# Optimization experiments

Measured on AMD Instinct MI355X. Metric: run time of the kernel, lower is better.

Reference implementation:

```python
import jax, jax.numpy as jnp
import numpy as np

N, E = 50000, 800000
S, V, RBF_DIM = 128, 16, 16
RBF_DMAX = 20.0
MSG_NORM = 10.0
EPS = 1e-8
DVH_M = V + 1            # message GVP: dim_vectors_in = V + 1 (edge direction appended), dim_h = max(17,16) = 17
FIN_M = S + RBF_DIM      # message GVP scalar input = node scalars + rbf(dist)
DVH_U = 2 * V            # update GVP: dim_vectors_in = 2V (node + aggregated), dim_h = 32
FIN_U = 2 * S


def _rbf(D):
    # [E] -> [E, RBF_DIM], matches torch _rbf with D_min=0, D_max=20, D_count=16
    D_mu = jnp.linspace(0.0, RBF_DMAX, RBF_DIM)
    D_sigma = RBF_DMAX / RBF_DIM
    return jnp.exp(-(((D[:, None] - D_mu[None, :]) / D_sigma) ** 2))


def _gvp(s, v, Wh, Wu, Wf, bf, Wg, bg):
    # s: [n, F_in], v: [n, V_in, 3]; faithful to GVP.forward with sigmoid vector gating
    Vh = jnp.einsum('nvc,vh->nhc', v, Wh)          # [n, H, 3]
    Vu = jnp.einsum('nhc,ho->noc', Vh, Wu)         # [n, V_out, 3]
    sh = jnp.sqrt(jnp.clip(jnp.sum(Vh * Vh, -1), EPS))  # _norm_no_nan
    feats_out = jax.nn.silu(jnp.concatenate([s, sh], -1) @ Wf + bf)
    gate = jax.nn.sigmoid(feats_out @ Wg + bg)[..., None]
    return feats_out, gate * Vu


def _gvp_layernorm(s, v, gamma, beta):
    mu = jnp.mean(s, -1, keepdims=True)
    var = jnp.mean((s - mu) ** 2, -1, keepdims=True)
    s_out = (s - mu) / jnp.sqrt(var + 1e-5) * gamma + beta
    vn = jnp.clip(jnp.sum(v * v, -1, keepdims=True), EPS)        # [N, V, 1]
    vn = jnp.sqrt(jnp.mean(vn, -2, keepdims=True) + 1e-5) + 1e-5  # [N, 1, 1]
    return s_out, v / vn


def setup_inputs() -> dict:
    key = jax.random.key(0)
    ks = jax.random.split(key, 14)
    rn = lambda k, shp, sc: (jax.random.normal(k, shp, dtype=jnp.float32) * sc)
    inp = {
        's': rn(ks[0], (N, S), 1.0),
        'v': rn(ks[1], (N, V, 3), 1.0),
        'x': rn(ks[2], (N, 3), 5.0),
        # message GVP params
        'Wh_m': rn(ks[3], (DVH_M, DVH_M), 1.0 / np.sqrt(DVH_M)),
        'Wu_m': rn(ks[4], (DVH_M, V), 1.0 / np.sqrt(DVH_M)),
        'Wf_m': rn(ks[5], (DVH_M + FIN_M, S), 1.0 / np.sqrt(DVH_M + FIN_M)),
        'bf_m': jnp.zeros((S,), jnp.float32),
        'Wg_m': rn(ks[6], (S, V), 1.0 / np.sqrt(S)),
        'bg_m': jnp.zeros((V,), jnp.float32),
        # update GVP params
        'Wh_u': rn(ks[7], (DVH_U, DVH_U), 1.0 / np.sqrt(DVH_U)),
        'Wu_u': rn(ks[8], (DVH_U, V), 1.0 / np.sqrt(DVH_U)),
        'Wf_u': rn(ks[9], (DVH_U + FIN_U, S), 1.0 / np.sqrt(DVH_U + FIN_U)),
        'bf_u': jnp.zeros((S,), jnp.float32),
        'Wg_u': rn(ks[10], (S, V), 1.0 / np.sqrt(S)),
        'bg_u': jnp.zeros((V,), jnp.float32),
        # layernorm
        'ln_g': jnp.ones((S,), jnp.float32),
        'ln_b': jnp.zeros((S,), jnp.float32),
        'edge_index': jax.random.randint(ks[11], (2, E), 0, N),
    }
    return inp


def reference(s, v, x, Wh_m, Wu_m, Wf_m, bf_m, Wg_m, bg_m,
              Wh_u, Wu_u, Wf_u, bf_u, Wg_u, bg_u, ln_g, ln_b, edge_index):
    src, dst = edge_index[0], edge_index[1]
    # gather + geometric edge features
    dx = x[dst] - x[src]                                   # [E, 3]
    dist = jnp.sqrt(jnp.clip(jnp.sum(dx * dx, -1), EPS))    # [E]
    unit = dx / dist[:, None]
    v_in = jnp.concatenate([v[src], unit[:, None, :]], 1)   # [E, V+1, 3]
    s_in = jnp.concatenate([s[src], _rbf(dist)], -1)        # [E, S+RBF]
    # message GVP
    ms, mv = _gvp(s_in, v_in, Wh_m, Wu_m, Wf_m, bf_m, Wg_m, bg_m)
    # scatter-reduce + message norm
    agg_s = jax.ops.segment_sum(ms, dst, num_segments=N) / MSG_NORM   # [N, S]
    agg_v = jax.ops.segment_sum(mv, dst, num_segments=N) / MSG_NORM   # [N, V, 3]
    # update GVP on concatenated node + aggregated messages
    us, uv = _gvp(jnp.concatenate([s, agg_s], -1), jnp.concatenate([v, agg_v], 1),
                  Wh_u, Wu_u, Wf_u, bf_u, Wg_u, bg_u)
    # residual + GVPLayerNorm
    return _gvp_layernorm(s + us, v + uv, ln_g, ln_b)
```

## Files before the change

kernel.cpp:

```cpp
#include <hip/hip_runtime.h>
#include <hip/hip_bf16.h>
#include <math.h>

#define N_NODES 50000
#define E_EDGES 800000
#define S_DIM 128
#define V_DIM 16
#define HM 17
#define KM 161
#define HU 32
#define KU 288

#define EB 32
#define LDA 164
#define NB 32
#define LDA2 292

__device__ __forceinline__ float bf2f(unsigned short u) {
    union { unsigned int i; float f; } w; w.i = ((unsigned int)u) << 16; return w.f;
}
__device__ __forceinline__ unsigned short f2bf(float f) {
    union { float f; unsigned int i; } w; w.f = f;
    unsigned int x = w.i;
    x += 0x7fff + ((x >> 16) & 1);
    return (unsigned short)(x >> 16);
}
__device__ __forceinline__ float silu_f(float x) { return x / (1.f + __expf(-x)); }
__device__ __forceinline__ float sigm_f(float x) { return 1.f / (1.f + __expf(-x)); }
__device__ __forceinline__ float ldf(const void* p, int i, int m) {
    if (m) return ((const float*)p)[i];
    return bf2f(((const unsigned short*)p)[i]);
}

__global__ void detect_kernel(const unsigned short* __restrict__ s_us,
                              int* __restrict__ flag) {
    int t = threadIdx.x;
    int huge = 0;
    for (int k = 0; k < 16; ++k) {
        unsigned short u = s_us[2 * (t + 64 * k)];
        int e = (u >> 7) & 0xFF;
        if (e > 140) huge = 1;
    }
    if (huge) atomicOr(flag, 1);
}

__global__ __launch_bounds__(256, 4) void edge_kernel(
    const void* sP, const void* vP, const void* xP,
    const void* WhP, const void* WuP, const void* WfP,
    const void* bfP, const void* WgP, const void* bgP,
    const int* __restrict__ ei,
    const int* __restrict__ flagp,
    float* __restrict__ agg_s,
    float* __restrict__ agg_v)
{
    __shared__ float A[EB * LDA];
    __shared__ float Bs[2048];
    __shared__ float WhWu[HM * 16];
    __shared__ float gates[EB * 16];
    __shared__ int srcb[EB], dstb[EB];

    const int t = threadIdx.x;
    const int e0 = blockIdx.x * EB;
    const int m = flagp[0];

    if (t < EB) {
        srcb[t] = ei[e0 + t];
        dstb[t] = ei[E_EDGES + e0 + t];
    }
    if (m) {
        const float* Wh = (const float*)WhP;
        const float* Wu = (const float*)WuP;
        for (int i = t; i < HM * HM; i += 256) gates[i] = Wh[i];
        for (int i = t; i < HM * 16; i += 256) Bs[1664 + i] = Wu[i];
    } else {
        const unsigned short* Wh = (const unsigned short*)WhP;
        const unsigned short* Wu = (const unsigned short*)WuP;
        for (int i = t; i < HM * HM; i += 256) gates[i] = bf2f(Wh[i]);
        for (int i = t; i < HM * 16; i += 256) Bs[1664 + i] = bf2f(Wu[i]);
    }
    __syncthreads();

    for (int idx = t; idx < HM * 16; idx += 256) {
        int vv = idx / 16, o = idx % 16;
        float acc = 0.f;
        for (int h = 0; h < HM; ++h)
            acc += gates[vv * HM + h] * Bs[1664 + h * 16 + o];
        WhWu[idx] = acc;
    }
    {
        int tj = t & 31, te = t >> 5;
        if (m) {
            const float* sF = (const float*)sP;
            for (int r = 0; r < 4; ++r) {
                int e = te + 8 * r;
                float4 u = *(const float4*)(sF + (size_t)srcb[e] * S_DIM + tj * 4);
                float* a = &A[e * LDA + tj * 4];
                a[0] = u.x; a[1] = u.y; a[2] = u.z; a[3] = u.w;
            }
        } else {
            const unsigned short* sU = (const unsigned short*)sP;
            for (int r = 0; r < 4; ++r) {
                int e = te + 8 * r;
                ushort4 u = *(const ushort4*)(sU + (size_t)srcb[e] * S_DIM + tj * 4);
                float* a = &A[e * LDA + tj * 4];
                a[0] = bf2f(u.x); a[1] = bf2f(u.y); a[2] = bf2f(u.z); a[3] = bf2f(u.w);
            }
        }
    }
    if (t < 128) {
        int e = t >> 2, q = t & 3;
        int src = srcb[e];
        float* vin = &Bs[e * 52 + q * 12];
        if (m) {
            const float* vp = (const float*)vP + (size_t)src * 48 + q * 12;
            for (int i = 0; i < 3; ++i) {
                float4 u = *(const float4*)(vp + i * 4);
                vin[i * 4 + 0] = u.x; vin[i * 4 + 1] = u.y;
                vin[i * 4 + 2] = u.z; vin[i * 4 + 3] = u.w;
            }
        } else {
            const unsigned short* vp = (const unsigned short*)vP + (size_t)src * 48 + q * 12;
            for (int i = 0; i < 3; ++i) {
                ushort4 u = *(const ushort4*)(vp + i * 4);
                vin[i * 4 + 0] = bf2f(u.x); vin[i * 4 + 1] = bf2f(u.y);
                vin[i * 4 + 2] = bf2f(u.z); vin[i * 4 + 3] = bf2f(u.w);
            }
        }
        if (q == 0) {
            int dst = dstb[e];
            float dxc[3]; float d2 = 0.f;
            for (int c = 0; c < 3; ++c) {
                float xs = ldf(xP, src * 3 + c, m);
                float xd = ldf(xP, dst * 3 + c, m);
                dxc[c] = xd - xs; d2 += dxc[c] * dxc[c];
            }
            float dist = sqrtf(fmaxf(d2, 1e-8f));
            float inv = 1.f / dist;
            for (int c = 0; c < 3; ++c) Bs[e * 52 + 48 + c] = dxc[c] * inv;
            for (int k = 0; k < 16; ++k) {
                float mu = (20.f / 15.f) * (float)k;
                float z = (dist - mu) * (1.f / 1.25f);
                A[e * LDA + 128 + k] = __expf(-z * z);
            }
        }
    }
    __syncthreads();

    for (int idx = t; idx < EB * HM; idx += 256) {
        int e = idx / HM, h = idx % HM;
        const float* vin = &Bs[e * 52];
        float vh0 = 0.f, vh1 = 0.f, vh2 = 0.f;
        for (int vv = 0; vv < HM; ++vv) {
            float w = gates[vv * HM + h];
            vh0 += vin[vv * 3 + 0] * w;
            vh1 += vin[vv * 3 + 1] * w;
            vh2 += vin[vv * 3 + 2] * w;
        }
        A[e * LDA + 144 + h] = sqrtf(fmaxf(vh0 * vh0 + vh1 * vh1 + vh2 * vh2, 1e-8f));
    }
    float vureg[6];
    for (int r = 0; r < 6; ++r) {
        int idx = t + 256 * r;
        int e = idx / 48, oc = idx % 48, o = oc / 3, c = oc % 3;
        const float* vin = &Bs[e * 52];
        float acc = 0.f;
        for (int vv = 0; vv < HM; ++vv)
            acc += vin[vv * 3 + c] * WhWu[vv * 16 + o];
        vureg[r] = acc;
    }
    __syncthreads();

    const int tj = t & 15, te = t >> 4;
    const int eb = te * 2;
    float acc[2][8];
    #pragma unroll
    for (int i = 0; i < 2; ++i)
        #pragma unroll
        for (int j = 0; j < 8; ++j) acc[i][j] = 0.f;

    for (int kk = 0; kk < KM; kk += 16) {
        int kmax = min(16, KM - kk);
        if (m) {
            const float* WfF = (const float*)WfP;
            for (int idx = t; idx < kmax * 32; idx += 256) {
                int kt = idx >> 5, col4 = (idx & 31) * 4;
                float4 u = *(const float4*)(WfF + (size_t)(kk + kt) * 128 + col4);
                float* b = &Bs[kt * 128 + col4];
                b[0] = u.x; b[1] = u.y; b[2] = u.z; b[3] = u.w;
            }
        } else {
            const unsigned short* WfU = (const unsigned short*)WfP;
            for (int idx = t; idx < kmax * 32; idx += 256) {
                int kt = idx >> 5, col4 = (idx & 31) * 4;
                ushort4 u = *(const ushort4*)(WfU + (size_t)(kk + kt) * 128 + col4);
                float* b = &Bs[kt * 128 + col4];
                b[0] = bf2f(u.x); b[1] = bf2f(u.y); b[2] = bf2f(u.z); b[3] = bf2f(u.w);
            }
        }
        __syncthreads();
        for (int kt = 0; kt < kmax; ++kt) {
            float a0 = A[(eb + 0) * LDA + kk + kt];
            float a1 = A[(eb + 1) * LDA + kk + kt];
            const float* brow = &Bs[kt * 128 + tj];
            #pragma unroll
            for (int jj = 0; jj < 8; ++jj) {
                float b = brow[16 * jj];
                acc[0][jj] += a0 * b; acc[1][jj] += a1 * b;
            }
        }
        __syncthreads();
    }
    float breg[8];
    #pragma unroll
    for (int jj = 0; jj < 8; ++jj) breg[jj] = ldf(bfP, tj + 16 * jj, m);
    #pragma unroll
    for (int i = 0; i < 2; ++i) {
        int e = eb + i;
        float* aout = &A[e * LDA];
        float* gp = &agg_s[(size_t)dstb[e] * S_DIM];
        #pragma unroll
        for (int jj = 0; jj < 8; ++jj) {
            int col = tj + 16 * jj;
            float f = silu_f(acc[i][jj] + breg[jj]);
            aout[col] = f;
            atomicAdd(&gp[col], f);
        }
    }
    __syncthreads();
    if (m) {
        const float* Wg = (const float*)WgP;
        for (int i = t; i < 2048; i += 256) Bs[i] = Wg[i];
    } else {
        const unsigned short* Wg = (const unsigned short*)WgP;
        for (int i = t; i < 2048; i += 256) Bs[i] = bf2f(Wg[i]);
    }
    __syncthreads();
    for (int r = 0; r < 2; ++r) {
        int idx = t + 256 * r;
        int e = idx / 16, o = idx % 16;
        const float* fe = &A[e * LDA];
        float g = ldf(bgP, o, m);
        for (int j = 0; j < S_DIM; ++j)
            g += fe[j] * Bs[j * 16 + o];
        gates[idx] = sigm_f(g);
    }
    __syncthreads();
    for (int r = 0; r < 6; ++r) {
        int idx = t + 256 * r;
        int e = idx / 48, oc = idx % 48, o = oc / 3;
        float mvv = vureg[r] * gates[e * 16 + o];
        atomicAdd(&agg_v[(size_t)dstb[e] * 48 + oc], mvv);
    }
}

__global__ __launch_bounds__(256) void node_kernel(
    const void* sP, const void* vP,
    const void* WhP, const void* WuP, const void* WfP,
    const void* bfP, const void* WgP, const void* bgP,
    const void* lngP, const void* lnbP,
    const int* __restrict__ flagp,
    const float* __restrict__ agg_s,
    const float* __restrict__ agg_v,
    void* outP)
{
    __shared__ float A2[NB * LDA2];
    __shared__ float Bs2[4096];
    __shared__ float WhWu2[HU * 16];
    __shared__ float gates2[NB * 16];
    __shared__ float WhS[HU * HU];
    __shared__ float mu_s[NB], rstd_s[NB], vn_s[NB];

    const int t = threadIdx.x;
    const int n0 = blockIdx.x * NB;
    const int m = flagp[0];

    if (m) {
        const float* Wh = (const float*)WhP;
        const float* Wu = (const float*)WuP;
        for (int i = t; i < HU * HU; i += 256) WhS[i] = Wh[i];
        for (int i = t; i < HU * 16; i += 256) gates2[i] = Wu[i];
    } else {
        const unsigned short* Wh = (const unsigned short*)WhP;
        const unsigned short* Wu = (const unsigned short*)WuP;
        for (int i = t; i < HU * HU; i += 256) WhS[i] = bf2f(Wh[i]);
        for (int i = t; i < HU * 16; i += 256) gates2[i] = bf2f(Wu[i]);
    }
    if (m) {
        const float* sF = (const float*)sP;
        for (int idx = t; idx < NB * 32; idx += 256) {
            int ni = idx >> 5, col4 = (idx & 31) * 4;
            int n = n0 + ni;
            float* a = &A2[ni * LDA2 + col4];
            if (n < N_NODES) {
                float4 u = *(const float4*)(sF + (size_t)n * 128 + col4);
                a[0] = u.x; a[1] = u.y; a[2] = u.z; a[3] = u.w;
            } else { a[0] = a[1] = a[2] = a[3] = 0.f; }
        }
    } else {
        const unsigned short* sU = (const unsigned short*)sP;
        for (int idx = t; idx < NB * 32; idx += 256) {
            int ni = idx >> 5, col4 = (idx & 31) * 4;
            int n = n0 + ni;
            float* a = &A2[ni * LDA2 + col4];
            if (n < N_NODES) {
                ushort4 u = *(const ushort4*)(sU + (size_t)n * 128 + col4);
                a[0] = bf2f(u.x); a[1] = bf2f(u.y); a[2] = bf2f(u.z); a[3] = bf2f(u.w);
            } else { a[0] = a[1] = a[2] = a[3] = 0.f; }
        }
    }
    for (int idx = t; idx < NB * 32; idx += 256) {
        int ni = idx >> 5, col4 = (idx & 31) * 4;
        int n = n0 + ni;
        float* a = &A2[ni * LDA2 + 128 + col4];
        if (n < N_NODES) {
            float4 u = *(const float4*)(agg_s + (size_t)n * 128 + col4);
            a[0] = u.x * 0.1f; a[1] = u.y * 0.1f; a[2] = u.z * 0.1f; a[3] = u.w * 0.1f;
        } else { a[0] = a[1] = a[2] = a[3] = 0.f; }
    }
    for (int idx = t; idx < NB * 96; idx += 256) {
        int ni = idx / 96, vc = idx % 96;
        int n = n0 + ni;
        float val = 0.f;
        if (n < N_NODES)
            val = (vc < 48) ? ldf(vP, n * 48 + vc, m)
                            : agg_v[(size_t)n * 48 + (vc - 48)] * 0.1f;
        Bs2[ni * 100 + vc] = val;
    }
    __syncthreads();
    for (int idx = t; idx < HU * 16; idx += 256) {
        int vv = idx / 16, o = idx % 16;
        float acc = 0.f;
        for (int h = 0; h < HU; ++h)
            acc += WhS[vv * HU + h] * gates2[h * 16 + o];
        WhWu2[idx] = acc;
    }
    for (int idx = t; idx < NB * HU; idx += 256) {
        int ni = idx / HU, h = idx % HU;
        const float* vc = &Bs2[ni * 100];
        float vh0 = 0.f, vh1 = 0.f, vh2 = 0.f;
        for (int vv = 0; vv < HU; ++vv) {
            float w = WhS[vv * HU + h];
            vh0 += vc[vv * 3 + 0] * w; vh1 += vc[vv * 3 + 1] * w; vh2 += vc[vv * 3 + 2] * w;
        }
        A2[ni * LDA2 + 256 + h] = sqrtf(fmaxf(vh0 * vh0 + vh1 * vh1 + vh2 * vh2, 1e-8f));
    }
    __syncthreads();
    float vureg[6];
    for (int r = 0; r < 6; ++r) {
        int idx = t + 256 * r;
        int ni = idx / 48, oc = idx % 48, o = oc / 3, c = oc % 3;
        const float* vc = &Bs2[ni * 100];
        float acc = 0.f;
        for (int vv = 0; vv < HU; ++vv)
            acc += vc[vv * 3 + c] * WhWu2[vv * 16 + o];
        vureg[r] = acc;
    }
    __syncthreads();

    const int tj = t & 15, tn = t >> 4;
    const int nb = tn * 2;
    float acc[2][8];
    #pragma unroll
    for (int i = 0; i < 2; ++i)
        #pragma unroll
        for (int j = 0; j < 8; ++j) acc[i][j] = 0.f;

    for (int kk = 0; kk < KU; kk += 32) {
        if (m) {
            const float* WfF = (const float*)WfP;
            for (int idx = t; idx < 32 * 32; idx += 256) {
                int kt = idx >> 5, col4 = (idx & 31) * 4;
                float4 u = *(const float4*)(WfF + (size_t)(kk + kt) * 128 + col4);
                float* b = &Bs2[kt * 128 + col4];
                b[0] = u.x; b[1] = u.y; b[2] = u.z; b[3] = u.w;
            }
        } else {
            const unsigned short* WfU = (const unsigned short*)WfP;
            for (int idx = t; idx < 32 * 32; idx += 256) {
                int kt = idx >> 5, col4 = (idx & 31) * 4;
                ushort4 u = *(const ushort4*)(WfU + (size_t)(kk + kt) * 128 + col4);
                float* b = &Bs2[kt * 128 + col4];
                b[0] = bf2f(u.x); b[1] = bf2f(u.y); b[2] = bf2f(u.z); b[3] = bf2f(u.w);
            }
        }
        __syncthreads();
        for (int kt = 0; kt < 32; ++kt) {
            float a0 = A2[(nb + 0) * LDA2 + kk + kt];
            float a1 = A2[(nb + 1) * LDA2 + kk + kt];
            const float* brow = &Bs2[kt * 128 + tj];
            #pragma unroll
            for (int jj = 0; jj < 8; ++jj) {
                float b = brow[16 * jj];
                acc[0][jj] += a0 * b; acc[1][jj] += a1 * b;
            }
        }
        __syncthreads();
    }
    float breg[8];
    #pragma unroll
    for (int jj = 0; jj < 8; ++jj) breg[jj] = ldf(bfP, tj + 16 * jj, m);
    #pragma unroll
    for (int i = 0; i < 2; ++i) {
        float* aout = &A2[(nb + i) * LDA2 + 128];
        #pragma unroll
        for (int jj = 0; jj < 8; ++jj)
            aout[tj + 16 * jj] = silu_f(acc[i][jj] + breg[jj]);
    }
    __syncthreads();
    if (m) {
        const float* Wg = (const float*)WgP;
        for (int i = t; i < 2048; i += 256) Bs2[i] = Wg[i];
    } else {
        const unsigned short* Wg = (const unsigned short*)WgP;
        for (int i = t; i < 2048; i += 256) Bs2[i] = bf2f(Wg[i]);
    }
    __syncthreads();
    for (int r = 0; r < 2; ++r) {
        int idx = t + 256 * r;
        int ni = idx / 16, o = idx % 16;
        const float* fe = &A2[ni * LDA2 + 128];
        float g = ldf(bgP, o, m);
        for (int j = 0; j < 128; ++j)
            g += fe[j] * Bs2[j * 16 + o];
        gates2[idx] = sigm_f(g);
    }
    __syncthreads();
    for (int r = 0; r < 6; ++r) {
        int idx = t + 256 * r;
        int ni = idx / 48, oc = idx % 48, o = oc / 3;
        int n = n0 + ni;
        float vres = 0.f;
        if (n < N_NODES)
            vres = ldf(vP, n * 48 + oc, m) + vureg[r] * gates2[ni * 16 + o];
        Bs2[ni * 48 + oc] = vres;
    }
    __syncthreads();
    if (t < NB) {
        const float* arow = &A2[t * LDA2];
        float sum = 0.f, sumsq = 0.f;
        for (int j = 0; j < 128; ++j) {
            float xr = arow[j] + arow[128 + j];
            sum += xr; sumsq += xr * xr;
        }
        float mu = sum * (1.f / 128.f);
        float var = sumsq * (1.f / 128.f) - mu * mu;
        mu_s[t] = mu;
        rstd_s[t] = rsqrtf(fmaxf(var, 0.f) + 1e-5f);
        const float* vr = &Bs2[t * 48];
        float accv = 0.f;
        for (int o = 0; o < 16; ++o) {
            float mm = vr[o*3]*vr[o*3] + vr[o*3+1]*vr[o*3+1] + vr[o*3+2]*vr[o*3+2];
            accv += fmaxf(mm, 1e-8f);
        }
        vn_s[t] = sqrtf(accv * (1.f / 16.f) + 1e-5f) + 1e-5f;
    }
    __syncthreads();
    float* outF = (float*)outP;
    unsigned short* outU = (unsigned short*)outP;
    for (int idx = t; idx < NB * 128; idx += 256) {
        int ni = idx >> 7, j = idx & 127;
        int n = n0 + ni;
        if (n < N_NODES) {
            float xr = A2[ni * LDA2 + j] + A2[ni * LDA2 + 128 + j];
            float o = (xr - mu_s[ni]) * rstd_s[ni] * ldf(lngP, j, m) + ldf(lnbP, j, m);
            if (m) outF[(size_t)n * 128 + j] = o;
            else   outU[(size_t)n * 128 + j] = f2bf(o);
        }
    }
    for (int idx = t; idx < NB * 48; idx += 256) {
        int ni = idx / 48, oc = idx % 48;
        int n = n0 + ni;
        if (n < N_NODES) {
            float o = Bs2[ni * 48 + oc] / vn_s[ni];
            if (m) outF[(size_t)N_NODES * 128 + (size_t)n * 48 + oc] = o;
            else   outU[(size_t)N_NODES * 128 + (size_t)n * 48 + oc] = f2bf(o);
        }
    }
}

extern "C" void kernel_launch(void* const* d_in, const int* in_sizes, int n_in,
                              void* d_out, int out_size, void* d_ws, size_t ws_size,
                              hipStream_t stream) {
    const int* ei = (const int*)d_in[17];

    int* flag = (int*)d_ws;
    float* agg_s = (float*)((char*)d_ws + 64);
    float* agg_v = agg_s + (size_t)N_NODES * 128;
    hipMemsetAsync(d_ws, 0, 64 + (size_t)N_NODES * (128 + 48) * sizeof(float), stream);

    detect_kernel<<<1, 64, 0, stream>>>((const unsigned short*)d_in[0], flag);

    edge_kernel<<<E_EDGES / EB, 256, 0, stream>>>(
        d_in[0], d_in[1], d_in[2], d_in[3], d_in[4], d_in[5],
        d_in[6], d_in[7], d_in[8], ei, flag, agg_s, agg_v);
    node_kernel<<<(N_NODES + NB - 1) / NB, 256, 0, stream>>>(
        d_in[0], d_in[1], d_in[9], d_in[10], d_in[11], d_in[12],
        d_in[13], d_in[14], d_in[15], d_in[16], flag,
        agg_s, agg_v, d_out);
}
```

Measured before the change: 2.498 ms.

## Sort edges by destination and pre-reduce runs before atomic scatter

Adds a counting-sort pass (histogram, single-block scan, scatter) that builds a permutation grouping edges by destination node. The edge kernel processes edges in that order and, per block, sums consecutive messages with the same destination in shared memory before issuing one atomicAdd per run. The aim is to cut global atomic traffic and contention on agg_s/agg_v. The cost is three extra kernels, a serial single-block scan over 50k nodes, and scattered src gathers, since edge order is now permuted.

After: 2.534 ms. Within noise of the previous version (+1.4%).

```diff
diff --git a/kernel.cpp b/kernel.cpp
--- a/kernel.cpp
+++ b/kernel.cpp
@@ -44,11 +44,53 @@
     if (huge) atomicOr(flag, 1);
 }
 
+__global__ void hist_kernel(const int* __restrict__ ei, int* __restrict__ cnt) {
+    int i = blockIdx.x * 256 + threadIdx.x;
+    if (i < E_EDGES) atomicAdd(&cnt[ei[E_EDGES + i]], 1);
+}
+
+__global__ void scan_kernel(int* __restrict__ cnt) {
+    __shared__ int buf[1024];
+    __shared__ int base_s;
+    const int t = threadIdx.x;
+    if (t == 0) base_s = 0;
+    __syncthreads();
+    for (int c0 = 0; c0 < N_NODES; c0 += 1024) {
+        int i = c0 + t;
+        int v = (i < N_NODES) ? cnt[i] : 0;
+        buf[t] = v;
+        __syncthreads();
+        for (int off = 1; off < 1024; off <<= 1) {
+            int tmp = (t >= off) ? buf[t - off] : 0;
+            __syncthreads();
+            buf[t] += tmp;
+            __syncthreads();
+        }
+        int base = base_s;
+        if (i < N_NODES) cnt[i] = base + buf[t] - v;
+        __syncthreads();
+        if (t == 0) base_s = base + buf[1023];
+        __syncthreads();
+    }
+}
+
+__global__ void scatter_kernel(const int* __restrict__ ei,
+                               int* __restrict__ cnt,
+                               int* __restrict__ perm) {
+    int i = blockIdx.x * 256 + threadIdx.x;
+    if (i < E_EDGES) {
+        int d = ei[E_EDGES + i];
+        int p = atomicAdd(&cnt[d], 1);
+        perm[p] = i;
+    }
+}
+
 __global__ __launch_bounds__(256, 4) void edge_kernel(
     const void* sP, const void* vP, const void* xP,
     const void* WhP, const void* WuP, const void* WfP,
     const void* bfP, const void* WgP, const void* bgP,
     const int* __restrict__ ei,
+    const int* __restrict__ perm,
     const int* __restrict__ flagp,
     float* __restrict__ agg_s,
     float* __restrict__ agg_v)
@@ -64,8 +106,9 @@
     const int m = flagp[0];
 
     if (t < EB) {
-        srcb[t] = ei[e0 + t];
-        dstb[t] = ei[E_EDGES + e0 + t];
+        int eid = perm[e0 + t];
+        srcb[t] = ei[eid];
+        dstb[t] = ei[E_EDGES + eid];
     }
     if (m) {
         const float* Wh = (const float*)WhP;
@@ -215,16 +258,10 @@
     for (int jj = 0; jj < 8; ++jj) breg[jj] = ldf(bfP, tj + 16 * jj, m);
     #pragma unroll
     for (int i = 0; i < 2; ++i) {
-        int e = eb + i;
-        float* aout = &A[e * LDA];
-        float* gp = &agg_s[(size_t)dstb[e] * S_DIM];
+        float* aout = &A[(eb + i) * LDA];
         #pragma unroll
-        for (int jj = 0; jj < 8; ++jj) {
-            int col = tj + 16 * jj;
-            float f = silu_f(acc[i][jj] + breg[jj]);
-            aout[col] = f;
-            atomicAdd(&gp[col], f);
-        }
+        for (int jj = 0; jj < 8; ++jj)
+            aout[tj + 16 * jj] = silu_f(acc[i][jj] + breg[jj]);
     }
     __syncthreads();
     if (m) {
@@ -248,8 +285,36 @@
     for (int r = 0; r < 6; ++r) {
         int idx = t + 256 * r;
         int e = idx / 48, oc = idx % 48, o = oc / 3;
-        float mvv = vureg[r] * gates[e * 16 + o];
-        atomicAdd(&agg_v[(size_t)dstb[e] * 48 + oc], mvv);
+        (void)oc;
+        Bs[idx] = vureg[r] * gates[e * 16 + o];
+    }
+    __syncthreads();
+    if (t < 176) {
+        float run = 0.f;
+        int cur = dstb[0];
+        if (t < 128) {
+            const int col = t;
+            for (int e = 0; e < EB; ++e) {
+                int d = dstb[e];
+                if (d != cur) {
+                    atomicAdd(&agg_s[(size_t)cur * S_DIM + col], run);
+                    run = 0.f; cur = d;
+                }
+                run += A[e * LDA + col];
+            }
+            atomicAdd(&agg_s[(size_t)cur * S_DIM + col], run);
+        } else {
+            const int oc = t - 128;
+            for (int e = 0; e < EB; ++e) {
+                int d = dstb[e];
+                if (d != cur) {
+                    atomicAdd(&agg_v[(size_t)cur * 48 + oc], run);
+                    run = 0.f; cur = d;
+                }
+                run += Bs[e * 48 + oc];
+            }
+            atomicAdd(&agg_v[(size_t)cur * 48 + oc], run);
+        }
     }
 }
 
@@ -484,15 +549,24 @@
     const int* ei = (const int*)d_in[17];
 
     int* flag = (int*)d_ws;
-    float* agg_s = (float*)((char*)d_ws + 64);
+    int* cnt = (int*)((char*)d_ws + 64);
+    float* agg_s = (float*)((char*)d_ws + 64 + 200000);
     float* agg_v = agg_s + (size_t)N_NODES * 128;
-    hipMemsetAsync(d_ws, 0, 64 + (size_t)N_NODES * (128 + 48) * sizeof(float), stream);
+    int* perm = (int*)(agg_v + (size_t)N_NODES * 48);
+
+    hipMemsetAsync(d_ws, 0,
+                   64 + 200000 + (size_t)N_NODES * (128 + 48) * sizeof(float),
+                   stream);
 
     detect_kernel<<<1, 64, 0, stream>>>((const unsigned short*)d_in[0], flag);
+
+    hist_kernel<<<(E_EDGES + 255) / 256, 256, 0, stream>>>(ei, cnt);
+    scan_kernel<<<1, 1024, 0, stream>>>(cnt);
+    scatter_kernel<<<(E_EDGES + 255) / 256, 256, 0, stream>>>(ei, cnt, perm);
 
     edge_kernel<<<E_EDGES / EB, 256, 0, stream>>>(
         d_in[0], d_in[1], d_in[2], d_in[3], d_in[4], d_in[5],
-        d_in[6], d_in[7], d_in[8], ei, flag, agg_s, agg_v);
+        d_in[6], d_in[7], d_in[8], ei, perm, flag, agg_s, agg_v);
     node_kernel<<<(N_NODES + NB - 1) / NB, 256, 0, stream>>>(
         d_in[0], d_in[1], d_in[9], d_in[10], d_in[11], d_in[12],
         d_in[13], d_in[14], d_in[15], d_in[16], flag,
```
